# Kernel tuning notes

Measured on AMD Instinct MI355X. Metric: run time of the kernel, lower is better.

## Reference

```python
import jax, jax.numpy as jnp
import numpy as np

B, L, N, F, H, HOR = 32, 12, 1024, 2, 128, 12


def setup_inputs() -> dict:
    key = jax.random.key(0)
    ks = jax.random.split(key, 9)
    x = jax.random.normal(ks[0], (B, L, N, F), dtype=jnp.float32)
    # A_phys: sparse-ish binary physical adjacency, then normalize_adj: add self-loops, row-normalize
    A_phys = (jax.random.uniform(ks[1], (N, N)) < 0.05).astype(jnp.float32)
    A = A_phys + jnp.eye(N, dtype=jnp.float32)
    A = A / (A.sum(axis=1, keepdims=True) + 1e-6)
    # GraphGRUCell params (single layer): lin_x: F -> 3H, lin_h: H -> 3H
    sx = 1.0 / np.sqrt(F)
    sh = 1.0 / np.sqrt(H)
    W_x = jax.random.uniform(ks[2], (F, 3 * H), minval=-sx, maxval=sx)
    b_x = jax.random.uniform(ks[3], (3 * H,), minval=-sx, maxval=sx)
    W_h = jax.random.uniform(ks[4], (H, 3 * H), minval=-sh, maxval=sh)
    b_h = jax.random.uniform(ks[5], (3 * H,), minval=-sh, maxval=sh)
    # head: H -> horizon
    W_head = jax.random.uniform(ks[6], (H, HOR), minval=-sh, maxval=sh)
    b_head = jax.random.uniform(ks[7], (HOR,), minval=-sh, maxval=sh)
    return {"x": x, "A": A, "W_x": W_x, "b_x": b_x, "W_h": W_h, "b_h": b_h,
            "W_head": W_head, "b_head": b_head}


def reference(x, A, W_x, b_x, W_h, b_h, W_head, b_head):
    Bv, Lv, Nv, Fv = x.shape
    Hv = W_h.shape[0]

    def step(h, xt):
        # graph aggregation of hidden state: [N,N] x [B,N,H] -> [B,N,H]
        Ah = jnp.einsum('ij,bjh->bih', A, h)
        x_gates = xt @ W_x + b_x          # [B,N,3H]
        h_gates = Ah @ W_h + b_h          # [B,N,3H]
        z_x, r_x, n_x = jnp.split(x_gates, 3, axis=-1)
        z_h, r_h, n_h = jnp.split(h_gates, 3, axis=-1)
        z = jax.nn.sigmoid(z_x + z_h)
        r = jax.nn.sigmoid(r_x + r_h)
        n = jnp.tanh(n_x + r * n_h)
        h_new = (1.0 - z) * n + z * h
        return h_new, None

    h0 = jnp.zeros((Bv, Nv, Hv), dtype=x.dtype)
    xs = jnp.moveaxis(x, 1, 0)  # [L,B,N,F]
    h, _ = jax.lax.scan(step, h0, xs)
    y = (h @ W_head + b_head).transpose(0, 2, 1)  # [B, horizon, N]
    return y
```

## Files before the change

### kernel.cpp

```cpp
#include <hip/hip_runtime.h>
#include <hip/hip_bf16.h>

#define BB 32
#define LL 12
#define NN 1024
#define HH 128
#define HORN 12
#define G3 384

typedef unsigned short u16;
typedef unsigned int u32;
typedef unsigned long long u64;
typedef __attribute__((ext_vector_type(8))) short short8;
typedef __attribute__((ext_vector_type(4))) float f32x4;

__device__ __forceinline__ u16 to_bf16(float f) {
    return __builtin_bit_cast(u16, __float2bfloat16(f));
}
__device__ __forceinline__ float bf_to_f(u32 bits) {
    return __builtin_bit_cast(float, bits << 16);
}
__device__ __forceinline__ void gl16(const u16* g, char* l) {
    __builtin_amdgcn_global_load_lds((const __attribute__((address_space(1))) u32*)g,
                                     (__attribute__((address_space(3))) u32*)l, 16, 0, 0);
}

__global__ void prep_abf(const float* __restrict__ A, u16* __restrict__ Abf) {
    int t = blockIdx.x * blockDim.x + threadIdx.x;
    float4 v = ((const float4*)A)[t];
    ushort4 o;
    o.x = to_bf16(v.x); o.y = to_bf16(v.y); o.z = to_bf16(v.z); o.w = to_bf16(v.w);
    ((ushort4*)Abf)[t] = o;
}

__global__ void prep_whT(const float* __restrict__ W_h, u16* __restrict__ whT) {
    int t = blockIdx.x * blockDim.x + threadIdx.x;
    if (t >= HH * G3) return;
    int c = t / HH, k = t % HH;
    whT[c * HH + k] = to_bf16(W_h[k * G3 + c]);
}

template <bool FIRST>
__global__ __launch_bounds__(256, 2) void gru_step(
    const u16* __restrict__ Abf, const u16* __restrict__ hT_old,
    u16* __restrict__ hT_new, const u16* __restrict__ whT,
    const float* __restrict__ x, const float* __restrict__ W_x,
    const float* __restrict__ b_x, const float* __restrict__ b_h, int t) {
    __shared__ __align__(16) char smem[65536];

    int bid = blockIdx.x;
    int swz = (bid & 7) * 64 + (bid >> 3);
    int b = swz >> 4;
    int i0 = (swz & 15) * 64;
    int tid = threadIdx.x;
    int w = tid >> 6, lane = tid & 63;
    int lcol = lane & 15, kgrp = lane >> 4;
    int wm = w >> 1, wn = w & 1;
    u32 swzl = (u32)((lcol & 7) << 4);

    u32 a_b = (u32)((wm * 32 + lcol) * 128);
    u32 b_b = (u32)(8192 + (wn * 64 + lcol) * 128);

    f32x4 acc[2][4];
#pragma unroll
    for (int m = 0; m < 2; ++m)
#pragma unroll
        for (int n = 0; n < 4; ++n) acc[m][n] = (f32x4){0.f, 0.f, 0.f, 0.f};

    u64 hreg[2][4] = {};

    if (!FIRST) {
        int lr3 = lane >> 3, lc8 = lane & 7;
        const u16* ag[2]; u32 al[2];
        const u16* bg[4]; u32 bl[4];
#pragma unroll
        for (int q = 0; q < 2; ++q) {
            int r = w * 16 + q * 8 + lr3;
            ag[q] = Abf + (size_t)(i0 + r) * 1024 + (lc8 ^ (r & 7)) * 8;
            al[q] = (u32)(w * 2048 + q * 1024);
        }
#pragma unroll
        for (int q = 0; q < 4; ++q) {
            int r = w * 32 + q * 8 + lr3;
            bg[q] = hT_old + (size_t)b * 131072 + (size_t)r * 1024 + (lc8 ^ (r & 7)) * 8;
            bl[q] = (u32)(8192 + w * 4096 + q * 1024);
        }

#pragma unroll
        for (int q = 0; q < 2; ++q) gl16(ag[q], smem + al[q]);
#pragma unroll
        for (int q = 0; q < 4; ++q) gl16(bg[q], smem + bl[q]);
#pragma unroll
        for (int q = 0; q < 2; ++q) gl16(ag[q] + 64, smem + 24576 + al[q]);
#pragma unroll
        for (int q = 0; q < 4; ++q) gl16(bg[q] + 64, smem + 24576 + bl[q]);

        int cstar = i0 >> 6;
        for (int c = 0; c < 16; ++c) {
            u32 sb = (u32)((c & 1) * 24576);
            if (c < 15) asm volatile("s_waitcnt vmcnt(6)" ::: "memory");
            else        asm volatile("s_waitcnt vmcnt(0)" ::: "memory");
            __builtin_amdgcn_s_barrier();
            __builtin_amdgcn_sched_barrier(0);

            if (c == cstar) {
#pragma unroll
                for (int sub = 0; sub < 2; ++sub) {
                    int hh = w * 32 + sub * 16 + lcol;
                    u32 rb = sb + 8192u + (u32)(hh * 128);
                    u32 sw = (u32)((hh & 7) << 4);
#pragma unroll
                    for (int rt = 0; rt < 4; ++rt)
                        hreg[sub][rt] = *(const u64*)(smem + rb + (((u32)(rt * 32 + kgrp * 8)) ^ sw));
                }
                asm volatile("s_waitcnt lgkmcnt(0)" ::: "memory");
                __builtin_amdgcn_sched_barrier(0);
            }

            __builtin_amdgcn_s_setprio(1);
#pragma unroll
            for (int ks = 0; ks < 2; ++ks) {
                u32 kb = ((u32)(ks * 64 + kgrp * 16)) ^ swzl;
                short8 a0 = *(const short8*)(smem + sb + a_b + kb);
                short8 a1 = *(const short8*)(smem + sb + a_b + 2048 + kb);
                short8 b0 = *(const short8*)(smem + sb + b_b + kb);
                short8 b1 = *(const short8*)(smem + sb + b_b + 2048 + kb);
                short8 b2 = *(const short8*)(smem + sb + b_b + 4096 + kb);
                short8 b3 = *(const short8*)(smem + sb + b_b + 6144 + kb);
                acc[0][0] = __builtin_amdgcn_mfma_f32_16x16x32_bf16(a0, b0, acc[0][0], 0, 0, 0);
                acc[0][1] = __builtin_amdgcn_mfma_f32_16x16x32_bf16(a0, b1, acc[0][1], 0, 0, 0);
                acc[0][2] = __builtin_amdgcn_mfma_f32_16x16x32_bf16(a0, b2, acc[0][2], 0, 0, 0);
                acc[0][3] = __builtin_amdgcn_mfma_f32_16x16x32_bf16(a0, b3, acc[0][3], 0, 0, 0);
                acc[1][0] = __builtin_amdgcn_mfma_f32_16x16x32_bf16(a1, b0, acc[1][0], 0, 0, 0);
                acc[1][1] = __builtin_amdgcn_mfma_f32_16x16x32_bf16(a1, b1, acc[1][1], 0, 0, 0);
                acc[1][2] = __builtin_amdgcn_mfma_f32_16x16x32_bf16(a1, b2, acc[1][2], 0, 0, 0);
                acc[1][3] = __builtin_amdgcn_mfma_f32_16x16x32_bf16(a1, b3, acc[1][3], 0, 0, 0);
            }
            __builtin_amdgcn_s_setprio(0);
            asm volatile("" ::: "memory");
            __builtin_amdgcn_s_barrier();
            if (c < 14) {
                int o = (c + 2) * 64;
#pragma unroll
                for (int q = 0; q < 2; ++q) gl16(ag[q] + o, smem + sb + al[q]);
#pragma unroll
                for (int q = 0; q < 4; ++q) gl16(bg[q] + o, smem + sb + bl[q]);
            }
        }
        asm volatile("" ::: "memory");
        __builtin_amdgcn_s_barrier();
    }

#pragma unroll
    for (int m = 0; m < 2; ++m)
#pragma unroll
        for (int n = 0; n < 4; ++n)
#pragma unroll
            for (int ri = 0; ri < 4; ++ri) {
                int row = wm * 32 + m * 16 + kgrp * 4 + ri;
                int col = wn * 64 + n * 16 + lcol;
                *(u16*)(smem + 49152 + row * 256 + (((u32)(2 * col)) ^ ((u32)(row & 7) << 4))) =
                    to_bf16(acc[m][n][ri]);
            }
    __syncthreads();

#pragma unroll
    for (int sub = 0; sub < 2; ++sub) {
        int hh = w * 32 + sub * 16 + lcol;
        short8 bw[3][4];
#pragma unroll
        for (int g = 0; g < 3; ++g)
#pragma unroll
            for (int ks = 0; ks < 4; ++ks)
                bw[g][ks] = *(const short8*)(whT + (size_t)(g * 128 + hh) * 128 + ks * 32 + kgrp * 8);

        f32x4 acc2[4][3];
#pragma unroll
        for (int rt = 0; rt < 4; ++rt)
#pragma unroll
            for (int g = 0; g < 3; ++g) acc2[rt][g] = (f32x4){0.f, 0.f, 0.f, 0.f};

        __builtin_amdgcn_s_setprio(1);
#pragma unroll
        for (int rt = 0; rt < 4; ++rt) {
            u32 ab2 = (u32)(49152 + (rt * 16 + lcol) * 256);
#pragma unroll
            for (int ks = 0; ks < 4; ++ks) {
                short8 a2 = *(const short8*)(smem + ab2 + (((u32)(ks * 64 + kgrp * 16)) ^ swzl));
                acc2[rt][0] = __builtin_amdgcn_mfma_f32_16x16x32_bf16(a2, bw[0][ks], acc2[rt][0], 0, 0, 0);
                acc2[rt][1] = __builtin_amdgcn_mfma_f32_16x16x32_bf16(a2, bw[1][ks], acc2[rt][1], 0, 0, 0);
                acc2[rt][2] = __builtin_amdgcn_mfma_f32_16x16x32_bf16(a2, bw[2][ks], acc2[rt][2], 0, 0, 0);
            }
        }
        __builtin_amdgcn_s_setprio(0);

        float bxz = b_x[hh], bxr = b_x[128 + hh], bxn = b_x[256 + hh];
        float bhz = b_h[hh], bhr = b_h[128 + hh], bhn = b_h[256 + hh];
        float wx0z = W_x[hh], wx0r = W_x[128 + hh], wx0n = W_x[256 + hh];
        float wx1z = W_x[G3 + hh], wx1r = W_x[G3 + 128 + hh], wx1n = W_x[G3 + 256 + hh];
#pragma unroll
        for (int rt = 0; rt < 4; ++rt) {
            u64 h4 = hreg[sub][rt];
#pragma unroll
            for (int ri = 0; ri < 4; ++ri) {
                int rl = rt * 16 + kgrp * 4 + ri;
                int i = i0 + rl;
                const float* xp = x + ((size_t)(b * LL + t) * NN + i) * 2;
                float x0 = xp[0], x1 = xp[1];
                float zin = acc2[rt][0][ri] + bhz + fmaf(x0, wx0z, fmaf(x1, wx1z, bxz));
                float rin = acc2[rt][1][ri] + bhr + fmaf(x0, wx0r, fmaf(x1, wx1r, bxr));
                float z = 1.f / (1.f + __expf(-zin));
                float rg = 1.f / (1.f + __expf(-rin));
                float nin = fmaf(rg, acc2[rt][2][ri] + bhn, fmaf(x0, wx0n, fmaf(x1, wx1n, bxn)));
                nin = fmaxf(nin, -40.f);
                float e = __expf(-2.f * nin);
                float n = (1.f - e) / (1.f + e);
                float hold = bf_to_f((u32)((h4 >> (16 * ri)) & 0xffffu));
                float hv = fmaf(z, hold - n, n);
                *(u16*)(smem + hh * 128 + (((u32)(2 * rl)) ^ ((u32)(hh & 7) << 4))) = to_bf16(hv);
            }
        }
    }
    __syncthreads();
#pragma unroll
    for (int c2 = 0; c2 < 4; ++c2) {
        int o = c2 * 4096 + tid * 16;
        int nr = o >> 7, cb = o & 127;
        uint4 v = *(const uint4*)(smem + nr * 128 + (((u32)cb) ^ ((u32)(nr & 7) << 4)));
        *(uint4*)((char*)(hT_new + (size_t)b * 131072 + (size_t)nr * 1024 + i0) + cb) = v;
    }
}

__global__ __launch_bounds__(256) void head_kernel(
    const u16* __restrict__ hT, const float* __restrict__ W_head,
    const float* __restrict__ b_head, float* __restrict__ out) {
    __shared__ float wl[HH * HORN];
    __shared__ float bl[HORN];
    int tid = threadIdx.x;
    for (int ix = tid; ix < HH * HORN; ix += 256) wl[ix] = W_head[ix];
    if (tid < HORN) bl[tid] = b_head[tid];
    __syncthreads();
    int blk = blockIdx.x;
    int b = blk >> 2;
    int i = (blk & 3) * 256 + tid;
    const u16* hp = hT + (size_t)b * 131072 + i;
    float acc[HORN];
#pragma unroll
    for (int hor = 0; hor < HORN; ++hor) acc[hor] = bl[hor];
    for (int hh = 0; hh < HH; ++hh) {
        float hv = bf_to_f((u32)hp[hh * 1024]);
#pragma unroll
        for (int hor = 0; hor < HORN; ++hor)
            acc[hor] = fmaf(hv, wl[hh * HORN + hor], acc[hor]);
    }
#pragma unroll
    for (int hor = 0; hor < HORN; ++hor)
        out[((size_t)b * HORN + hor) * NN + i] = acc[hor];
}

extern "C" void kernel_launch(void* const* d_in, const int* in_sizes, int n_in,
                              void* d_out, int out_size, void* d_ws, size_t ws_size,
                              hipStream_t stream) {
    const float* x = (const float*)d_in[0];
    const float* A = (const float*)d_in[1];
    const float* W_x = (const float*)d_in[2];
    const float* b_x = (const float*)d_in[3];
    const float* W_h = (const float*)d_in[4];
    const float* b_h = (const float*)d_in[5];
    const float* W_head = (const float*)d_in[6];
    const float* b_head = (const float*)d_in[7];
    float* out = (float*)d_out;
    char* ws = (char*)d_ws;

    u16* hT0 = (u16*)(ws + 0);
    u16* hT1 = (u16*)(ws + 8388608);
    u16* Abf = (u16*)(ws + 16777216);
    u16* whT = (u16*)(ws + 18874368);

    prep_abf<<<1024, 256, 0, stream>>>(A, Abf);
    prep_whT<<<(HH * G3 + 255) / 256, 256, 0, stream>>>(W_h, whT);

    gru_step<true><<<512, 256, 0, stream>>>(Abf, hT1, hT0, whT, x, W_x, b_x, b_h, 0);
    u16* hTo = hT0; u16* hTn = hT1;
    for (int t = 1; t < LL; ++t) {
        gru_step<false><<<512, 256, 0, stream>>>(Abf, hTo, hTn, whT, x, W_x, b_x, b_h, t);
        u16* tmp = hTo; hTo = hTn; hTn = tmp;
    }
    head_kernel<<<BB * 4, 256, 0, stream>>>(hTo, W_head, b_head, out);
}
```

Measured before the change: 306.3 us.

## Fuse all GRU timesteps and head into one persistent kernel with per-batch counters

Replaces the twelve per-timestep launches and the separate head kernel with a single persistent kernel. Blocks sharing a batch index synchronise through per-(batch,timestep) atomic counters in the workspace, with a release fence before each increment. Each timestep writes h to its own buffer, so there is no write-after-read hazard across blocks. The A tile prefetch is issued before the spin-wait, gate constants are hoisted out of the time loop, and the head projection is computed from shared memory in the final step. This removes launch gaps and the final h round trip, but relies on all 512 blocks being co-resident (2 per CU) to avoid deadlock and adds a memset launch.

```diff
diff --git a/kernel.cpp b/kernel.cpp
--- a/kernel.cpp
+++ b/kernel.cpp
@@ -25,6 +25,11 @@
                                      (__attribute__((address_space(3))) u32*)l, 16, 0, 0);
 }
 
+#define HT_STRIDE 8454144ull
+#define ABF_OFF   (11ull * HT_STRIDE)
+#define WHT_OFF   (ABF_OFF + 2097152ull)
+#define CTR_OFF   (WHT_OFF + 98304ull)
+
 __global__ void prep_abf(const float* __restrict__ A, u16* __restrict__ Abf) {
     int t = blockIdx.x * blockDim.x + threadIdx.x;
     float4 v = ((const float4*)A)[t];
@@ -40,222 +45,250 @@
     whT[c * HH + k] = to_bf16(W_h[k * G3 + c]);
 }
 
-template <bool FIRST>
-__global__ __launch_bounds__(256, 2) void gru_step(
-    const u16* __restrict__ Abf, const u16* __restrict__ hT_old,
-    u16* __restrict__ hT_new, const u16* __restrict__ whT,
+__global__ __launch_bounds__(256, 2) void fused_dcrnn(
     const float* __restrict__ x, const float* __restrict__ W_x,
-    const float* __restrict__ b_x, const float* __restrict__ b_h, int t) {
+    const float* __restrict__ b_x, const float* __restrict__ b_h,
+    const float* __restrict__ W_head, const float* __restrict__ b_head,
+    float* __restrict__ out, char* __restrict__ ws) {
     __shared__ __align__(16) char smem[65536];
 
-    int bid = blockIdx.x;
+    const u16* Abf = (const u16*)(ws + ABF_OFF);
+    const u16* whT = (const u16*)(ws + WHT_OFF);
+    int* counters = (int*)(ws + CTR_OFF);
+
+    int bid = blockIdx.x, tid = threadIdx.x;
+
     int swz = (bid & 7) * 64 + (bid >> 3);
     int b = swz >> 4;
     int i0 = (swz & 15) * 64;
-    int tid = threadIdx.x;
     int w = tid >> 6, lane = tid & 63;
     int lcol = lane & 15, kgrp = lane >> 4;
     int wm = w >> 1, wn = w & 1;
     u32 swzl = (u32)((lcol & 7) << 4);
-
     u32 a_b = (u32)((wm * 32 + lcol) * 128);
     u32 b_b = (u32)(8192 + (wn * 64 + lcol) * 128);
 
-    f32x4 acc[2][4];
-#pragma unroll
-    for (int m = 0; m < 2; ++m)
-#pragma unroll
-        for (int n = 0; n < 4; ++n) acc[m][n] = (f32x4){0.f, 0.f, 0.f, 0.f};
-
-    u64 hreg[2][4] = {};
-
-    if (!FIRST) {
-        int lr3 = lane >> 3, lc8 = lane & 7;
-        const u16* ag[2]; u32 al[2];
-        const u16* bg[4]; u32 bl[4];
-#pragma unroll
-        for (int q = 0; q < 2; ++q) {
-            int r = w * 16 + q * 8 + lr3;
-            ag[q] = Abf + (size_t)(i0 + r) * 1024 + (lc8 ^ (r & 7)) * 8;
-            al[q] = (u32)(w * 2048 + q * 1024);
+    int lr3 = lane >> 3, lc8 = lane & 7;
+    const u16* ag[2]; u32 al[2];
+    int brows[4]; u32 blo[4]; u32 bcol[4];
+#pragma unroll
+    for (int q = 0; q < 2; ++q) {
+        int r = w * 16 + q * 8 + lr3;
+        ag[q] = Abf + (size_t)(i0 + r) * 1024 + (lc8 ^ (r & 7)) * 8;
+        al[q] = (u32)(w * 2048 + q * 1024);
+    }
+#pragma unroll
+    for (int q = 0; q < 4; ++q) {
+        brows[q] = w * 32 + q * 8 + lr3;
+        blo[q] = (u32)(8192 + w * 4096 + q * 1024);
+        bcol[q] = (u32)((lc8 ^ (brows[q] & 7)) * 8);
+    }
+
+    float ebx[2][3], ebh[2][3], ew0[2][3], ew1[2][3];
+#pragma unroll
+    for (int sub = 0; sub < 2; ++sub) {
+        int hh = w * 32 + sub * 16 + lcol;
+#pragma unroll
+        for (int g = 0; g < 3; ++g) {
+            ebx[sub][g] = b_x[g * 128 + hh];
+            ebh[sub][g] = b_h[g * 128 + hh];
+            ew0[sub][g] = W_x[g * 128 + hh];
+            ew1[sub][g] = W_x[G3 + g * 128 + hh];
         }
-#pragma unroll
-        for (int q = 0; q < 4; ++q) {
-            int r = w * 32 + q * 8 + lr3;
-            bg[q] = hT_old + (size_t)b * 131072 + (size_t)r * 1024 + (lc8 ^ (r & 7)) * 8;
-            bl[q] = (u32)(8192 + w * 4096 + q * 1024);
-        }
-
-#pragma unroll
-        for (int q = 0; q < 2; ++q) gl16(ag[q], smem + al[q]);
-#pragma unroll
-        for (int q = 0; q < 4; ++q) gl16(bg[q], smem + bl[q]);
-#pragma unroll
-        for (int q = 0; q < 2; ++q) gl16(ag[q] + 64, smem + 24576 + al[q]);
-#pragma unroll
-        for (int q = 0; q < 4; ++q) gl16(bg[q] + 64, smem + 24576 + bl[q]);
-
-        int cstar = i0 >> 6;
-        for (int c = 0; c < 16; ++c) {
-            u32 sb = (u32)((c & 1) * 24576);
-            if (c < 15) asm volatile("s_waitcnt vmcnt(6)" ::: "memory");
-            else        asm volatile("s_waitcnt vmcnt(0)" ::: "memory");
-            __builtin_amdgcn_s_barrier();
-            __builtin_amdgcn_sched_barrier(0);
-
-            if (c == cstar) {
-#pragma unroll
-                for (int sub = 0; sub < 2; ++sub) {
-                    int hh = w * 32 + sub * 16 + lcol;
-                    u32 rb = sb + 8192u + (u32)(hh * 128);
-                    u32 sw = (u32)((hh & 7) << 4);
-#pragma unroll
-                    for (int rt = 0; rt < 4; ++rt)
-                        hreg[sub][rt] = *(const u64*)(smem + rb + (((u32)(rt * 32 + kgrp * 8)) ^ sw));
-                }
-                asm volatile("s_waitcnt lgkmcnt(0)" ::: "memory");
+    }
+
+    for (int t = 0; t < LL; ++t) {
+        const u16* hTo = (const u16*)(ws + (size_t)(t - 1) * HT_STRIDE);
+        u16* hTn = (u16*)(ws + (size_t)t * HT_STRIDE);
+
+        f32x4 acc[2][4];
+#pragma unroll
+        for (int m = 0; m < 2; ++m)
+#pragma unroll
+            for (int n = 0; n < 4; ++n) acc[m][n] = (f32x4){0.f, 0.f, 0.f, 0.f};
+        u64 hreg[2][4] = {{0, 0, 0, 0}, {0, 0, 0, 0}};
+
+        if (t > 0) {
+            const u16* bg[4];
+#pragma unroll
+            for (int q = 0; q < 4; ++q)
+                bg[q] = hTo + (size_t)b * 131072 + (size_t)brows[q] * 1024 + bcol[q];
+
+#pragma unroll
+            for (int q = 0; q < 2; ++q) gl16(ag[q], smem + al[q]);
+#pragma unroll
+            for (int q = 0; q < 2; ++q) gl16(ag[q] + 64, smem + 24576 + al[q]);
+
+            if (tid == 0) {
+                const int* cp = counters + b * LL + (t - 1);
+                while (__hip_atomic_load(cp, __ATOMIC_RELAXED, __HIP_MEMORY_SCOPE_AGENT) < 16)
+                    __builtin_amdgcn_s_sleep(4);
+            }
+            __syncthreads();
+
+#pragma unroll
+            for (int q = 0; q < 4; ++q) gl16(bg[q], smem + blo[q]);
+#pragma unroll
+            for (int q = 0; q < 4; ++q) gl16(bg[q] + 64, smem + 24576 + blo[q]);
+
+            int cstar = i0 >> 6;
+            for (int c = 0; c < 16; ++c) {
+                u32 sb = (u32)((c & 1) * 24576);
+                if (c == 0)      asm volatile("s_waitcnt vmcnt(4)" ::: "memory");
+                else if (c < 15) asm volatile("s_waitcnt vmcnt(6)" ::: "memory");
+                else             asm volatile("s_waitcnt vmcnt(0)" ::: "memory");
+                __builtin_amdgcn_s_barrier();
                 __builtin_amdgcn_sched_barrier(0);
-            }
-
-            __builtin_amdgcn_s_setprio(1);
-#pragma unroll
-            for (int ks = 0; ks < 2; ++ks) {
-                u32 kb = ((u32)(ks * 64 + kgrp * 16)) ^ swzl;
-                short8 a0 = *(const short8*)(smem + sb + a_b + kb);
-                short8 a1 = *(const short8*)(smem + sb + a_b + 2048 + kb);
-                short8 b0 = *(const short8*)(smem + sb + b_b + kb);
-                short8 b1 = *(const short8*)(smem + sb + b_b + 2048 + kb);
-                short8 b2 = *(const short8*)(smem + sb + b_b + 4096 + kb);
-                short8 b3 = *(const short8*)(smem + sb + b_b + 6144 + kb);
-                acc[0][0] = __builtin_amdgcn_mfma_f32_16x16x32_bf16(a0, b0, acc[0][0], 0, 0, 0);
-                acc[0][1] = __builtin_amdgcn_mfma_f32_16x16x32_bf16(a0, b1, acc[0][1], 0, 0, 0);
-                acc[0][2] = __builtin_amdgcn_mfma_f32_16x16x32_bf16(a0, b2, acc[0][2], 0, 0, 0);
-                acc[0][3] = __builtin_amdgcn_mfma_f32_16x16x32_bf16(a0, b3, acc[0][3], 0, 0, 0);
-                acc[1][0] = __builtin_amdgcn_mfma_f32_16x16x32_bf16(a1, b0, acc[1][0], 0, 0, 0);
-                acc[1][1] = __builtin_amdgcn_mfma_f32_16x16x32_bf16(a1, b1, acc[1][1], 0, 0, 0);
-                acc[1][2] = __builtin_amdgcn_mfma_f32_16x16x32_bf16(a1, b2, acc[1][2], 0, 0, 0);
-                acc[1][3] = __builtin_amdgcn_mfma_f32_16x16x32_bf16(a1, b3, acc[1][3], 0, 0, 0);
-            }
-            __builtin_amdgcn_s_setprio(0);
+
+                if (c == cstar) {
+#pragma unroll
+                    for (int sub = 0; sub < 2; ++sub) {
+                        int hh = w * 32 + sub * 16 + lcol;
+                        u32 rb = sb + 8192u + (u32)(hh * 128);
+                        u32 sw = (u32)((hh & 7) << 4);
+#pragma unroll
+                        for (int rt = 0; rt < 4; ++rt)
+                            hreg[sub][rt] = *(const u64*)(smem + rb + (((u32)(rt * 32 + kgrp * 8)) ^ sw));
+                    }
+                    asm volatile("s_waitcnt lgkmcnt(0)" ::: "memory");
+                    __builtin_amdgcn_sched_barrier(0);
+                }
+
+                __builtin_amdgcn_s_setprio(1);
+#pragma unroll
+                for (int ks = 0; ks < 2; ++ks) {
+                    u32 kb = ((u32)(ks * 64 + kgrp * 16)) ^ swzl;
+                    short8 a0 = *(const short8*)(smem + sb + a_b + kb);
+                    short8 a1 = *(const short8*)(smem + sb + a_b + 2048 + kb);
+                    short8 b0 = *(const short8*)(smem + sb + b_b + kb);
+                    short8 b1 = *(const short8*)(smem + sb + b_b + 2048 + kb);
+                    short8 b2 = *(const short8*)(smem + sb + b_b + 4096 + kb);
+                    short8 b3 = *(const short8*)(smem + sb + b_b + 6144 + kb);
+                    acc[0][0] = __builtin_amdgcn_mfma_f32_16x16x32_bf16(a0, b0, acc[0][0], 0, 0, 0);
+                    acc[0][1] = __builtin_amdgcn_mfma_f32_16x16x32_bf16(a0, b1, acc[0][1], 0, 0, 0);
+                    acc[0][2] = __builtin_amdgcn_mfma_f32_16x16x32_bf16(a0, b2, acc[0][2], 0, 0, 0);
+                    acc[0][3] = __builtin_amdgcn_mfma_f32_16x16x32_bf16(a0, b3, acc[0][3], 0, 0, 0);
+                    acc[1][0] = __builtin_amdgcn_mfma_f32_16x16x32_bf16(a1, b0, acc[1][0], 0, 0, 0);
+                    acc[1][1] = __builtin_amdgcn_mfma_f32_16x16x32_bf16(a1, b1, acc[1][1], 0, 0, 0);
+                    acc[1][2] = __builtin_amdgcn_mfma_f32_16x16x32_bf16(a1, b2, acc[1][2], 0, 0, 0);
+                    acc[1][3] = __builtin_amdgcn_mfma_f32_16x16x32_bf16(a1, b3, acc[1][3], 0, 0, 0);
+                }
+                __builtin_amdgcn_s_setprio(0);
+                asm volatile("" ::: "memory");
+                __builtin_amdgcn_s_barrier();
+                if (c < 14) {
+                    int o = (c + 2) * 64;
+#pragma unroll
+                    for (int q = 0; q < 2; ++q) gl16(ag[q] + o, smem + sb + al[q]);
+#pragma unroll
+                    for (int q = 0; q < 4; ++q) gl16(bg[q] + o, smem + sb + blo[q]);
+                }
+            }
             asm volatile("" ::: "memory");
             __builtin_amdgcn_s_barrier();
-            if (c < 14) {
-                int o = (c + 2) * 64;
-#pragma unroll
-                for (int q = 0; q < 2; ++q) gl16(ag[q] + o, smem + sb + al[q]);
-#pragma unroll
-                for (int q = 0; q < 4; ++q) gl16(bg[q] + o, smem + sb + bl[q]);
-            }
         }
-        asm volatile("" ::: "memory");
-        __builtin_amdgcn_s_barrier();
-    }
-
-#pragma unroll
-    for (int m = 0; m < 2; ++m)
-#pragma unroll
-        for (int n = 0; n < 4; ++n)
-#pragma unroll
-            for (int ri = 0; ri < 4; ++ri) {
-                int row = wm * 32 + m * 16 + kgrp * 4 + ri;
-                int col = wn * 64 + n * 16 + lcol;
-                *(u16*)(smem + 49152 + row * 256 + (((u32)(2 * col)) ^ ((u32)(row & 7) << 4))) =
-                    to_bf16(acc[m][n][ri]);
-            }
-    __syncthreads();
-
-#pragma unroll
-    for (int sub = 0; sub < 2; ++sub) {
-        int hh = w * 32 + sub * 16 + lcol;
-        short8 bw[3][4];
-#pragma unroll
-        for (int g = 0; g < 3; ++g)
-#pragma unroll
-            for (int ks = 0; ks < 4; ++ks)
-                bw[g][ks] = *(const short8*)(whT + (size_t)(g * 128 + hh) * 128 + ks * 32 + kgrp * 8);
-
-        f32x4 acc2[4][3];
-#pragma unroll
-        for (int rt = 0; rt < 4; ++rt)
-#pragma unroll
-            for (int g = 0; g < 3; ++g) acc2[rt][g] = (f32x4){0.f, 0.f, 0.f, 0.f};
-
-        __builtin_amdgcn_s_setprio(1);
-#pragma unroll
-        for (int rt = 0; rt < 4; ++rt) {
-            u32 ab2 = (u32)(49152 + (rt * 16 + lcol) * 256);
-#pragma unroll
-            for (int ks = 0; ks < 4; ++ks) {
-                short8 a2 = *(const short8*)(smem + ab2 + (((u32)(ks * 64 + kgrp * 16)) ^ swzl));
-                acc2[rt][0] = __builtin_amdgcn_mfma_f32_16x16x32_bf16(a2, bw[0][ks], acc2[rt][0], 0, 0, 0);
-                acc2[rt][1] = __builtin_amdgcn_mfma_f32_16x16x32_bf16(a2, bw[1][ks], acc2[rt][1], 0, 0, 0);
-                acc2[rt][2] = __builtin_amdgcn_mfma_f32_16x16x32_bf16(a2, bw[2][ks], acc2[rt][2], 0, 0, 0);
+
+#pragma unroll
+        for (int m = 0; m < 2; ++m)
+#pragma unroll
+            for (int n = 0; n < 4; ++n)
+#pragma unroll
+                for (int ri = 0; ri < 4; ++ri) {
+                    int row = wm * 32 + m * 16 + kgrp * 4 + ri;
+                    int col = wn * 64 + n * 16 + lcol;
+                    *(u16*)(smem + 49152 + row * 256 + (((u32)(2 * col)) ^ ((u32)(row & 7) << 4))) =
+                        to_bf16(acc[m][n][ri]);
+                }
+        __syncthreads();
+
+#pragma unroll
+        for (int sub = 0; sub < 2; ++sub) {
+            int hh = w * 32 + sub * 16 + lcol;
+            short8 bw[3][4];
+#pragma unroll
+            for (int g = 0; g < 3; ++g)
+#pragma unroll
+                for (int ks = 0; ks < 4; ++ks)
+                    bw[g][ks] = *(const short8*)(whT + (size_t)(g * 128 + hh) * 128 + ks * 32 + kgrp * 8);
+
+            f32x4 acc2[4][3];
+#pragma unroll
+            for (int rt = 0; rt < 4; ++rt)
+#pragma unroll
+                for (int g = 0; g < 3; ++g) acc2[rt][g] = (f32x4){0.f, 0.f, 0.f, 0.f};
+
+            __builtin_amdgcn_s_setprio(1);
+#pragma unroll
+            for (int rt = 0; rt < 4; ++rt) {
+                u32 ab2 = (u32)(49152 + (rt * 16 + lcol) * 256);
+#pragma unroll
+                for (int ks = 0; ks < 4; ++ks) {
+                    short8 a2 = *(const short8*)(smem + ab2 + (((u32)(ks * 64 + kgrp * 16)) ^ swzl));
+                    acc2[rt][0] = __builtin_amdgcn_mfma_f32_16x16x32_bf16(a2, bw[0][ks], acc2[rt][0], 0, 0, 0);
+                    acc2[rt][1] = __builtin_amdgcn_mfma_f32_16x16x32_bf16(a2, bw[1][ks], acc2[rt][1], 0, 0, 0);
+                    acc2[rt][2] = __builtin_amdgcn_mfma_f32_16x16x32_bf16(a2, bw[2][ks], acc2[rt][2], 0, 0, 0);
+                }
+            }
+            __builtin_amdgcn_s_setprio(0);
+
+#pragma unroll
+            for (int rt = 0; rt < 4; ++rt) {
+                u64 h4 = hreg[sub][rt];
+#pragma unroll
+                for (int ri = 0; ri < 4; ++ri) {
+                    int rl = rt * 16 + kgrp * 4 + ri;
+                    int i = i0 + rl;
+                    const float* xp = x + ((size_t)(b * LL + t) * NN + i) * 2;
+                    float x0 = xp[0], x1 = xp[1];
+                    float zin = acc2[rt][0][ri] + ebh[sub][0] + fmaf(x0, ew0[sub][0], fmaf(x1, ew1[sub][0], ebx[sub][0]));
+                    float rin = acc2[rt][1][ri] + ebh[sub][1] + fmaf(x0, ew0[sub][1], fmaf(x1, ew1[sub][1], ebx[sub][1]));
+                    float z = 1.f / (1.f + __expf(-zin));
+                    float rg = 1.f / (1.f + __expf(-rin));
+                    float nin = fmaf(rg, acc2[rt][2][ri] + ebh[sub][2], fmaf(x0, ew0[sub][2], fmaf(x1, ew1[sub][2], ebx[sub][2])));
+                    nin = fmaxf(nin, -40.f);
+                    float e = __expf(-2.f * nin);
+                    float n = (1.f - e) / (1.f + e);
+                    float hold = bf_to_f((u32)((h4 >> (16 * ri)) & 0xffffu));
+                    float hv = fmaf(z, hold - n, n);
+                    *(u16*)(smem + hh * 128 + (((u32)(2 * rl)) ^ ((u32)(hh & 7) << 4))) = to_bf16(hv);
+                }
             }
         }
-        __builtin_amdgcn_s_setprio(0);
-
-        float bxz = b_x[hh], bxr = b_x[128 + hh], bxn = b_x[256 + hh];
-        float bhz = b_h[hh], bhr = b_h[128 + hh], bhn = b_h[256 + hh];
-        float wx0z = W_x[hh], wx0r = W_x[128 + hh], wx0n = W_x[256 + hh];
-        float wx1z = W_x[G3 + hh], wx1r = W_x[G3 + 128 + hh], wx1n = W_x[G3 + 256 + hh];
-#pragma unroll
-        for (int rt = 0; rt < 4; ++rt) {
-            u64 h4 = hreg[sub][rt];
-#pragma unroll
-            for (int ri = 0; ri < 4; ++ri) {
-                int rl = rt * 16 + kgrp * 4 + ri;
-                int i = i0 + rl;
-                const float* xp = x + ((size_t)(b * LL + t) * NN + i) * 2;
-                float x0 = xp[0], x1 = xp[1];
-                float zin = acc2[rt][0][ri] + bhz + fmaf(x0, wx0z, fmaf(x1, wx1z, bxz));
-                float rin = acc2[rt][1][ri] + bhr + fmaf(x0, wx0r, fmaf(x1, wx1r, bxr));
-                float z = 1.f / (1.f + __expf(-zin));
-                float rg = 1.f / (1.f + __expf(-rin));
-                float nin = fmaf(rg, acc2[rt][2][ri] + bhn, fmaf(x0, wx0n, fmaf(x1, wx1n, bxn)));
-                nin = fmaxf(nin, -40.f);
-                float e = __expf(-2.f * nin);
-                float n = (1.f - e) / (1.f + e);
-                float hold = bf_to_f((u32)((h4 >> (16 * ri)) & 0xffffu));
-                float hv = fmaf(z, hold - n, n);
-                *(u16*)(smem + hh * 128 + (((u32)(2 * rl)) ^ ((u32)(hh & 7) << 4))) = to_bf16(hv);
-            }
+        __syncthreads();
+
+        if (t < LL - 1) {
+#pragma unroll
+            for (int c2 = 0; c2 < 4; ++c2) {
+                int o = c2 * 4096 + tid * 16;
+                int nr = o >> 7, cb = o & 127;
+                uint4 v = *(const uint4*)(smem + nr * 128 + (((u32)cb) ^ ((u32)(nr & 7) << 4)));
+                *(uint4*)((char*)(hTn + (size_t)b * 131072 + (size_t)nr * 1024 + i0) + cb) = v;
+            }
+            asm volatile("s_waitcnt vmcnt(0)" ::: "memory");
+            __syncthreads();
+            if (tid == 0) {
+                __builtin_amdgcn_fence(__ATOMIC_RELEASE, "agent");
+                __hip_atomic_fetch_add(counters + b * LL + t, 1, __ATOMIC_RELAXED, __HIP_MEMORY_SCOPE_AGENT);
+            }
+        } else {
+            float* wl = (float*)(smem + 49152);
+            float* blh = (float*)(smem + 55296);
+            for (int ix = tid; ix < HH * HORN; ix += 256) wl[ix] = W_head[ix];
+            if (tid < HORN) blh[tid] = b_head[tid];
+            __syncthreads();
+            int il = tid & 63, hg = tid >> 6;
+            float a0 = blh[hg], a1 = blh[hg + 4], a2 = blh[hg + 8];
+            for (int hh = 0; hh < 128; ++hh) {
+                float hv = bf_to_f((u32)*(const u16*)(smem + hh * 128 + (((u32)(2 * il)) ^ ((u32)(hh & 7) << 4))));
+                a0 = fmaf(hv, wl[hh * HORN + hg], a0);
+                a1 = fmaf(hv, wl[hh * HORN + hg + 4], a1);
+                a2 = fmaf(hv, wl[hh * HORN + hg + 8], a2);
+            }
+            out[(size_t)(b * HORN + hg) * NN + i0 + il] = a0;
+            out[(size_t)(b * HORN + hg + 4) * NN + i0 + il] = a1;
+            out[(size_t)(b * HORN + hg + 8) * NN + i0 + il] = a2;
         }
     }
-    __syncthreads();
-#pragma unroll
-    for (int c2 = 0; c2 < 4; ++c2) {
-        int o = c2 * 4096 + tid * 16;
-        int nr = o >> 7, cb = o & 127;
-        uint4 v = *(const uint4*)(smem + nr * 128 + (((u32)cb) ^ ((u32)(nr & 7) << 4)));
-        *(uint4*)((char*)(hT_new + (size_t)b * 131072 + (size_t)nr * 1024 + i0) + cb) = v;
-    }
-}
-
-__global__ __launch_bounds__(256) void head_kernel(
-    const u16* __restrict__ hT, const float* __restrict__ W_head,
-    const float* __restrict__ b_head, float* __restrict__ out) {
-    __shared__ float wl[HH * HORN];
-    __shared__ float bl[HORN];
-    int tid = threadIdx.x;
-    for (int ix = tid; ix < HH * HORN; ix += 256) wl[ix] = W_head[ix];
-    if (tid < HORN) bl[tid] = b_head[tid];
-    __syncthreads();
-    int blk = blockIdx.x;
-    int b = blk >> 2;
-    int i = (blk & 3) * 256 + tid;
-    const u16* hp = hT + (size_t)b * 131072 + i;
-    float acc[HORN];
-#pragma unroll
-    for (int hor = 0; hor < HORN; ++hor) acc[hor] = bl[hor];
-    for (int hh = 0; hh < HH; ++hh) {
-        float hv = bf_to_f((u32)hp[hh * 1024]);
-#pragma unroll
-        for (int hor = 0; hor < HORN; ++hor)
-            acc[hor] = fmaf(hv, wl[hh * HORN + hor], acc[hor]);
-    }
-#pragma unroll
-    for (int hor = 0; hor < HORN; ++hor)
-        out[((size_t)b * HORN + hor) * NN + i] = acc[hor];
 }
 
 extern "C" void kernel_launch(void* const* d_in, const int* in_sizes, int n_in,
@@ -272,19 +305,12 @@
     float* out = (float*)d_out;
     char* ws = (char*)d_ws;
 
-    u16* hT0 = (u16*)(ws + 0);
-    u16* hT1 = (u16*)(ws + 8388608);
-    u16* Abf = (u16*)(ws + 16777216);
-    u16* whT = (u16*)(ws + 18874368);
+    u16* Abf = (u16*)(ws + ABF_OFF);
+    u16* whT = (u16*)(ws + WHT_OFF);
 
     prep_abf<<<1024, 256, 0, stream>>>(A, Abf);
     prep_whT<<<(HH * G3 + 255) / 256, 256, 0, stream>>>(W_h, whT);
-
-    gru_step<true><<<512, 256, 0, stream>>>(Abf, hT1, hT0, whT, x, W_x, b_x, b_h, 0);
-    u16* hTo = hT0; u16* hTn = hT1;
-    for (int t = 1; t < LL; ++t) {
-        gru_step<false><<<512, 256, 0, stream>>>(Abf, hTo, hTn, whT, x, W_x, b_x, b_h, t);
-        u16* tmp = hTo; hTo = hTn; hTn = tmp;
-    }
-    head_kernel<<<BB * 4, 256, 0, stream>>>(hTo, W_head, b_head, out);
-}
+    hipMemsetAsync(ws + CTR_OFF, 0, BB * LL * sizeof(int), stream);
+
+    fused_dcrnn<<<512, 256, 0, stream>>>(x, W_x, b_x, b_h, W_head, b_head, out, ws);
+}
```

Measured after the change: 660.6 us. +115.6%, slower.

## Fuse head projection into last GRU step and shrink LDS footprint

Applied to the files above, without the earlier changes.

The final GRU step gains a LAST template variant that computes the horizon head directly from the new hidden tile held in shared memory. This removes the separate head kernel launch and the last global hidden-state write and read. Shared memory is cut from 64KB to 48KB by placing the aggregated tile over the staging buffers, and launch bounds are raised to 3 blocks per CU. The tighter bound may limit registers and cause spills, and with only 512 blocks the extra occupancy may not be used.

```diff
diff --git a/kernel.cpp b/kernel.cpp
--- a/kernel.cpp
+++ b/kernel.cpp
@@ -40,13 +40,15 @@
     whT[c * HH + k] = to_bf16(W_h[k * G3 + c]);
 }
 
-template <bool FIRST>
-__global__ __launch_bounds__(256, 2) void gru_step(
+template <bool FIRST, bool LAST>
+__global__ __launch_bounds__(256, 3) void gru_step(
     const u16* __restrict__ Abf, const u16* __restrict__ hT_old,
     u16* __restrict__ hT_new, const u16* __restrict__ whT,
     const float* __restrict__ x, const float* __restrict__ W_x,
-    const float* __restrict__ b_x, const float* __restrict__ b_h, int t) {
-    __shared__ __align__(16) char smem[65536];
+    const float* __restrict__ b_x, const float* __restrict__ b_h,
+    const float* __restrict__ W_head, const float* __restrict__ b_head,
+    float* __restrict__ out, int t) {
+    __shared__ __align__(16) char smem[49152];
 
     int bid = blockIdx.x;
     int swz = (bid & 7) * 64 + (bid >> 3);
@@ -57,7 +59,6 @@
     int lcol = lane & 15, kgrp = lane >> 4;
     int wm = w >> 1, wn = w & 1;
     u32 swzl = (u32)((lcol & 7) << 4);
-
     u32 a_b = (u32)((wm * 32 + lcol) * 128);
     u32 b_b = (u32)(8192 + (wn * 64 + lcol) * 128);
 
@@ -66,8 +67,7 @@
     for (int m = 0; m < 2; ++m)
 #pragma unroll
         for (int n = 0; n < 4; ++n) acc[m][n] = (f32x4){0.f, 0.f, 0.f, 0.f};
-
-    u64 hreg[2][4] = {};
+    u64 hreg[2][4] = {{0, 0, 0, 0}, {0, 0, 0, 0}};
 
     if (!FIRST) {
         int lr3 = lane >> 3, lc8 = lane & 7;
@@ -159,7 +159,7 @@
             for (int ri = 0; ri < 4; ++ri) {
                 int row = wm * 32 + m * 16 + kgrp * 4 + ri;
                 int col = wn * 64 + n * 16 + lcol;
-                *(u16*)(smem + 49152 + row * 256 + (((u32)(2 * col)) ^ ((u32)(row & 7) << 4))) =
+                *(u16*)(smem + row * 256 + (((u32)(2 * col)) ^ ((u32)(row & 7) << 4))) =
                     to_bf16(acc[m][n][ri]);
             }
     __syncthreads();
@@ -183,7 +183,7 @@
         __builtin_amdgcn_s_setprio(1);
 #pragma unroll
         for (int rt = 0; rt < 4; ++rt) {
-            u32 ab2 = (u32)(49152 + (rt * 16 + lcol) * 256);
+            u32 ab2 = (u32)((rt * 16 + lcol) * 256);
 #pragma unroll
             for (int ks = 0; ks < 4; ++ks) {
                 short8 a2 = *(const short8*)(smem + ab2 + (((u32)(ks * 64 + kgrp * 16)) ^ swzl));
@@ -217,45 +217,38 @@
                 float n = (1.f - e) / (1.f + e);
                 float hold = bf_to_f((u32)((h4 >> (16 * ri)) & 0xffffu));
                 float hv = fmaf(z, hold - n, n);
-                *(u16*)(smem + hh * 128 + (((u32)(2 * rl)) ^ ((u32)(hh & 7) << 4))) = to_bf16(hv);
+                *(u16*)(smem + 16384 + hh * 128 + (((u32)(2 * rl)) ^ ((u32)(hh & 7) << 4))) = to_bf16(hv);
             }
         }
     }
     __syncthreads();
-#pragma unroll
-    for (int c2 = 0; c2 < 4; ++c2) {
-        int o = c2 * 4096 + tid * 16;
-        int nr = o >> 7, cb = o & 127;
-        uint4 v = *(const uint4*)(smem + nr * 128 + (((u32)cb) ^ ((u32)(nr & 7) << 4)));
-        *(uint4*)((char*)(hT_new + (size_t)b * 131072 + (size_t)nr * 1024 + i0) + cb) = v;
-    }
-}
-
-__global__ __launch_bounds__(256) void head_kernel(
-    const u16* __restrict__ hT, const float* __restrict__ W_head,
-    const float* __restrict__ b_head, float* __restrict__ out) {
-    __shared__ float wl[HH * HORN];
-    __shared__ float bl[HORN];
-    int tid = threadIdx.x;
-    for (int ix = tid; ix < HH * HORN; ix += 256) wl[ix] = W_head[ix];
-    if (tid < HORN) bl[tid] = b_head[tid];
-    __syncthreads();
-    int blk = blockIdx.x;
-    int b = blk >> 2;
-    int i = (blk & 3) * 256 + tid;
-    const u16* hp = hT + (size_t)b * 131072 + i;
-    float acc[HORN];
-#pragma unroll
-    for (int hor = 0; hor < HORN; ++hor) acc[hor] = bl[hor];
-    for (int hh = 0; hh < HH; ++hh) {
-        float hv = bf_to_f((u32)hp[hh * 1024]);
-#pragma unroll
-        for (int hor = 0; hor < HORN; ++hor)
-            acc[hor] = fmaf(hv, wl[hh * HORN + hor], acc[hor]);
-    }
-#pragma unroll
-    for (int hor = 0; hor < HORN; ++hor)
-        out[((size_t)b * HORN + hor) * NN + i] = acc[hor];
+
+    if (!LAST) {
+#pragma unroll
+        for (int c2 = 0; c2 < 4; ++c2) {
+            int o = c2 * 4096 + tid * 16;
+            int nr = o >> 7, cb = o & 127;
+            uint4 v = *(const uint4*)(smem + 16384 + nr * 128 + (((u32)cb) ^ ((u32)(nr & 7) << 4)));
+            *(uint4*)((char*)(hT_new + (size_t)b * 131072 + (size_t)nr * 1024 + i0) + cb) = v;
+        }
+    } else {
+        float* wl = (float*)(smem + 32768);
+        float* blh = (float*)(smem + 38912);
+        for (int ix = tid; ix < HH * HORN; ix += 256) wl[ix] = W_head[ix];
+        if (tid < HORN) blh[tid] = b_head[tid];
+        __syncthreads();
+        int il = tid & 63, hg = tid >> 6;
+        float a0 = blh[hg], a1 = blh[hg + 4], a2 = blh[hg + 8];
+        for (int hh = 0; hh < 128; ++hh) {
+            float hv = bf_to_f((u32)*(const u16*)(smem + 16384 + hh * 128 + (((u32)(2 * il)) ^ ((u32)(hh & 7) << 4))));
+            a0 = fmaf(hv, wl[hh * HORN + hg], a0);
+            a1 = fmaf(hv, wl[hh * HORN + hg + 4], a1);
+            a2 = fmaf(hv, wl[hh * HORN + hg + 8], a2);
+        }
+        out[(size_t)(b * HORN + hg) * NN + i0 + il] = a0;
+        out[(size_t)(b * HORN + hg + 4) * NN + i0 + il] = a1;
+        out[(size_t)(b * HORN + hg + 8) * NN + i0 + il] = a2;
+    }
 }
 
 extern "C" void kernel_launch(void* const* d_in, const int* in_sizes, int n_in,
@@ -280,11 +273,14 @@
     prep_abf<<<1024, 256, 0, stream>>>(A, Abf);
     prep_whT<<<(HH * G3 + 255) / 256, 256, 0, stream>>>(W_h, whT);
 
-    gru_step<true><<<512, 256, 0, stream>>>(Abf, hT1, hT0, whT, x, W_x, b_x, b_h, 0);
+    gru_step<true, false><<<512, 256, 0, stream>>>(Abf, hT1, hT0, whT, x, W_x, b_x, b_h,
+                                                   W_head, b_head, out, 0);
     u16* hTo = hT0; u16* hTn = hT1;
-    for (int t = 1; t < LL; ++t) {
-        gru_step<false><<<512, 256, 0, stream>>>(Abf, hTo, hTn, whT, x, W_x, b_x, b_h, t);
+    for (int t = 1; t < LL - 1; ++t) {
+        gru_step<false, false><<<512, 256, 0, stream>>>(Abf, hTo, hTn, whT, x, W_x, b_x, b_h,
+                                                        W_head, b_head, out, t);
         u16* tmp = hTo; hTo = hTn; hTn = tmp;
     }
-    head_kernel<<<BB * 4, 256, 0, stream>>>(hTo, W_head, b_head, out);
-}
+    gru_step<false, true><<<512, 256, 0, stream>>>(Abf, hTo, hTn, whT, x, W_x, b_x, b_h,
+                                                   W_head, b_head, out, LL - 1);
+}
```

New measurement: 307.3 us. Within noise of the previous version (+0.3%).
